# Optimization experiments

Measured on AMD Instinct MI355X. Metric: run time of the kernel, lower is better.

The kernel has to match this reference:

```python
import jax, jax.numpy as jnp
import numpy as np

N, E, SEQ, IN, HID, OUT = 2048, 65536, 5, 32, 64, 16
EPS = 1e-5


def setup_inputs() -> dict:
    ks = jax.random.split(jax.random.key(0), 16)
    def w(k, shape):
        return jax.random.normal(k, shape, jnp.float32) / np.float32(np.sqrt(shape[0]))
    z = lambda n: jnp.zeros((n,), jnp.float32)
    return dict(
        x=jax.random.normal(ks[0], (SEQ, N, IN), jnp.float32),
        edge_weight=jax.random.uniform(ks[1], (E,), jnp.float32),
        Wcz=w(ks[2], (IN, HID)), bcz=z(HID), Wlz=w(ks[3], (2 * HID, HID)), blz=z(HID),
        Wcr=w(ks[4], (IN, HID)), bcr=z(HID), Wlr=w(ks[5], (2 * HID, HID)), blr=z(HID),
        Wch=w(ks[6], (IN, HID)), bch=z(HID), Wlh=w(ks[7], (2 * HID, HID)), blh=z(HID),
        Wred=w(ks[8], (SEQ * HID, HID)), bred=z(HID),
        Wc1=w(ks[9], (HID, HID)), bc1=z(HID), Wc2=w(ks[10], (HID, HID)), bc2=z(HID),
        g1=jnp.ones((HID,), jnp.float32), be1=z(HID),
        g2=jnp.ones((HID,), jnp.float32), be2=z(HID),
        Wout=w(ks[11], (HID, OUT)), bout=z(OUT),
        Wi1=w(ks[12], (2 * HID, HID)), bi1=z(HID),
        Wi2=w(ks[13], (HID, 1)), bi2=z(1),
        edge_index=jax.random.randint(ks[14], (2, E), 0, N),
    )


def _layer_norm(h, g, b):
    mu = jnp.mean(h, -1, keepdims=True)
    var = jnp.mean((h - mu) ** 2, -1, keepdims=True)
    return (h - mu) * jax.lax.rsqrt(var + EPS) * g + b


def _forward(x, edge_weight, Wcz, bcz, Wlz, blz, Wcr, bcr, Wlr, blr,
             Wch, bch, Wlh, blh, Wred, bred, Wc1, bc1, Wc2, bc2,
             g1, be1, g2, be2, Wout, bout, Wi1, bi1, Wi2, bi2, edge_index):
    src, dst = edge_index[0], edge_index[1]
    # GCN symmetric normalization with self-loops (weight 1.0); shared by all convs.
    deg = jax.ops.segment_sum(edge_weight, dst, num_segments=N) + 1.0
    dinv = jax.lax.rsqrt(deg)
    norm = dinv[src] * edge_weight * dinv[dst]  # [E]
    dself = dinv * dinv                          # [N] self-loop coefficient

    def gcn(h, W, b):
        hw = h @ W
        agg = jax.ops.segment_sum(norm[:, None] * hw[src], dst, num_segments=N)
        return agg + dself[:, None] * hw + b

    # TGCN per timestep. The original passes no hidden state, so H resets to 0
    # each call: H_t = (1 - Z) * tanh(candidate); reset gate R is multiplied by
    # H=0 and has no effect (its params get zero gradient, matching torch).
    hs = []
    for t in range(SEQ):  # SEQ=5, fixed small loop
        Zg = jax.nn.sigmoid(gcn(x[t], Wcz, bcz) @ Wlz[:HID] + blz)
        Ht = jnp.tanh(gcn(x[t], Wch, bch) @ Wlh[:HID] + blh)
        hs.append((1.0 - Zg) * Ht)
    h = jnp.stack(hs, axis=1).reshape(N, SEQ * HID)
    h = h @ Wred + bred
    emb = h  # intermediate embeddings for the interaction predictor
    h = gcn(h, Wc1, bc1)
    h = jax.nn.relu(_layer_norm(h, g1, be1))  # dropout = identity in eval
    h = gcn(h, Wc2, bc2)
    h = jax.nn.relu(_layer_norm(h, g2, be2))
    node_pred = h @ Wout + bout
    # InteractionPredictor: cat([e_i, e_j]) @ Wi1 == e_i @ Wi1[:H] + e_j @ Wi1[H:]
    a = emb @ Wi1[:HID]
    bj = emb @ Wi1[HID:]
    hp = jax.nn.relu(a[:, None, :] + bj[None, :, :] + bi1)  # [N, N, HID]
    scores = (hp @ Wi2)[..., 0] + bi2[0]                     # [N, N]
    return node_pred, scores


def reference(x, edge_index, edge_weight, Wcz, bcz, Wlz, blz, Wcr, bcr, Wlr, blr,
              Wch, bch, Wlh, blh, Wred, bred, Wc1, bc1, Wc2, bc2,
              g1, be1, g2, be2, Wout, bout, Wi1, bi1, Wi2, bi2):
    return _forward(x, edge_weight, Wcz, bcz, Wlz, blz, Wcr, bcr, Wlr, blr,
                    Wch, bch, Wlh, blh, Wred, bred, Wc1, bc1, Wc2, bc2,
                    g1, be1, g2, be2, Wout, bout, Wi1, bi1, Wi2, bi2, edge_index)
```

## Files before the change

### kernel.cpp

```cpp
#include <hip/hip_runtime.h>
#include <math.h>

#define N_NODES 2048
#define N_EDGES 65536
#define SEQL 5
#define IN_F 32
#define HID 64
#define OUT_F 16
#define LN_EPS 1e-5f

__global__ __launch_bounds__(256) void k_deg_wcomb(
        const int* __restrict__ ei, const float* __restrict__ ew,
        const float* __restrict__ Wcz, const float* __restrict__ Wlz,
        const float* __restrict__ bcz, const float* __restrict__ blz,
        const float* __restrict__ Wch, const float* __restrict__ Wlh,
        const float* __restrict__ bch, const float* __restrict__ blh,
        float* __restrict__ deg, int* __restrict__ cnt,
        float* __restrict__ Wzp, float* __restrict__ Whp, float* __restrict__ bUV){
    int b = blockIdx.x, t = threadIdx.x;
    if (b < 256){
        int e = b * 256 + t;
        int d = ei[N_EDGES + e];
        atomicAdd(&deg[d], ew[e]);
        atomicAdd(&cnt[d], 1);
    } else {
        const float* Wc = (b == 256) ? Wcz : Wch;
        const float* Wl = (b == 256) ? Wlz : Wlh;
        const float* bc = (b == 256) ? bcz : bch;
        const float* bl = (b == 256) ? blz : blh;
        float* Wp = (b == 256) ? Wzp : Whp;
        for (int idx = t; idx < IN_F*HID; idx += 256){
            int i = idx >> 6, f = idx & 63;
            float s = 0.f;
            #pragma unroll 8
            for (int k = 0; k < HID; ++k) s += Wc[i*HID+k] * Wl[k*HID+f];
            Wp[idx] = s;
        }
        if (t < HID){
            float s = bl[t];
            for (int k = 0; k < HID; ++k) s += bc[k] * Wl[k*HID+t];
            bUV[(b-256)*HID + t] = s;
        }
    }
}

__global__ __launch_bounds__(1024) void k_scan(
        const float* __restrict__ deg, const int* __restrict__ cnt,
        int* __restrict__ rowptr, float* __restrict__ dinv, float* __restrict__ dself,
        int* __restrict__ fill){
    __shared__ int sc[1024];
    int t = threadIdx.x;
    int c0 = cnt[2*t], c1 = cnt[2*t+1];
    int ts = c0 + c1;
    sc[t] = ts;
    __syncthreads();
    for (int off = 1; off < 1024; off <<= 1){
        int v = (t >= off) ? sc[t - off] : 0;
        __syncthreads();
        sc[t] += v;
        __syncthreads();
    }
    int exc = sc[t] - ts;
    rowptr[2*t]   = exc;
    rowptr[2*t+1] = exc + c0;
    if (t == 1023) rowptr[N_NODES] = sc[t];
    float i0 = 1.f / sqrtf(deg[2*t] + 1.f);
    float i1 = 1.f / sqrtf(deg[2*t+1] + 1.f);
    dinv[2*t] = i0;     dinv[2*t+1] = i1;
    dself[2*t] = i0*i0; dself[2*t+1] = i1*i1;
    fill[2*t] = 0;      fill[2*t+1] = 0;
}

__global__ void k_csr(const int* __restrict__ ei, const float* __restrict__ ew,
                      const float* __restrict__ dinv, const int* __restrict__ rowptr,
                      int* __restrict__ fill, float2* __restrict__ cedge){
    int e = blockIdx.x * 256 + threadIdx.x;
    if (e < N_EDGES){
        int s = ei[e], d = ei[N_EDGES + e];
        int pos = rowptr[d] + atomicAdd(&fill[d], 1);
        float2 v;
        v.x = __int_as_float(s);
        v.y = dinv[s] * ew[e] * dinv[d];
        cedge[pos] = v;
    }
}

__global__ __launch_bounds__(320) void k_gate(const float* __restrict__ x,
        const float* __restrict__ dself, const int* __restrict__ rowptr,
        const float2* __restrict__ cedge,
        const float* __restrict__ bUV, const float* __restrict__ Wzp, const float* __restrict__ Whp,
        const float* __restrict__ Wred, const float* __restrict__ bred,
        const float* __restrict__ Wi1, const float* __restrict__ bi1, const float* __restrict__ Wc1,
        float* __restrict__ ag, float* __restrict__ bjp, float* __restrict__ hw1){
    int n = blockIdx.x;
    int tid = threadIdx.x;
    __shared__ float part[40*SEQL*IN_F];
    __shared__ float axs[SEQL][IN_F];
    __shared__ float hs[SEQL][HID];
    __shared__ float pw[SEQL][HID];
    __shared__ float hemb[HID];
    const int slot = tid >> 3, fl = tid & 7;
    const int f = tid & 63, t = tid >> 6;
    int beg = rowptr[n], end = rowptr[n+1];
    const float4* X4 = (const float4*)x;
    float4 a0 = {0,0,0,0}, a1 = {0,0,0,0}, a2 = {0,0,0,0}, a3 = {0,0,0,0}, a4 = {0,0,0,0};
    for (int p = beg + slot; p < end; p += 40){
        float2 ed = cedge[p];
        int s = __float_as_int(ed.x); float c = ed.y;
        float4 x0 = X4[(0*N_NODES + s)*8 + fl];
        float4 x1 = X4[(1*N_NODES + s)*8 + fl];
        float4 x2 = X4[(2*N_NODES + s)*8 + fl];
        float4 x3 = X4[(3*N_NODES + s)*8 + fl];
        float4 x4v= X4[(4*N_NODES + s)*8 + fl];
        a0.x += c*x0.x; a0.y += c*x0.y; a0.z += c*x0.z; a0.w += c*x0.w;
        a1.x += c*x1.x; a1.y += c*x1.y; a1.z += c*x1.z; a1.w += c*x1.w;
        a2.x += c*x2.x; a2.y += c*x2.y; a2.z += c*x2.z; a2.w += c*x2.w;
        a3.x += c*x3.x; a3.y += c*x3.y; a3.z += c*x3.z; a3.w += c*x3.w;
        a4.x += c*x4v.x; a4.y += c*x4v.y; a4.z += c*x4v.z; a4.w += c*x4v.w;
    }
    *(float4*)&part[(slot*SEQL + 0)*IN_F + fl*4] = a0;
    *(float4*)&part[(slot*SEQL + 1)*IN_F + fl*4] = a1;
    *(float4*)&part[(slot*SEQL + 2)*IN_F + fl*4] = a2;
    *(float4*)&part[(slot*SEQL + 3)*IN_F + fl*4] = a3;
    *(float4*)&part[(slot*SEQL + 4)*IN_F + fl*4] = a4;
    __syncthreads();
    if (tid < SEQL*IN_F){
        int tt = tid >> 5, ff = tid & 31;
        float s = dself[n] * x[(tt*N_NODES + n)*IN_F + ff];
        #pragma unroll 8
        for (int sl = 0; sl < 40; ++sl) s += part[(sl*SEQL + tt)*IN_F + ff];
        axs[tt][ff] = s;
    }
    __syncthreads();
    {
        float zz = bUV[f], hh = bUV[HID + f];
        #pragma unroll
        for (int i = 0; i < IN_F; ++i){
            float a = axs[t][i];
            zz += a * Wzp[i*HID + f];
            hh += a * Whp[i*HID + f];
        }
        float z = 1.f / (1.f + expf(-zz));
        hs[t][f] = (1.f - z) * tanhf(hh);
    }
    __syncthreads();
    {   float pp = 0.f;
        #pragma unroll
        for (int k = 0; k < HID; ++k) pp += hs[t][k] * Wred[(t*HID + k)*HID + f];
        pw[t][f] = pp;
    }
    __syncthreads();
    if (tid < HID){
        float hr = bred[tid];
        #pragma unroll
        for (int t2 = 0; t2 < SEQL; ++t2) hr += pw[t2][tid];
        hemb[tid] = hr;
    }
    __syncthreads();
    if (t < 3){
        const float* W = (t == 0) ? Wi1 : (t == 1) ? (Wi1 + HID*HID) : Wc1;
        float acc = (t == 1) ? bi1[f] : 0.f;
        #pragma unroll
        for (int k = 0; k < HID; ++k) acc += hemb[k] * W[k*HID + f];
        float* O = (t == 0) ? ag : (t == 1) ? bjp : hw1;
        O[n*HID + f] = acc;
    }
}

__global__ __launch_bounds__(512) void k_gcn1(
        const float* __restrict__ hw1, const float* __restrict__ dself,
        const int* __restrict__ rowptr, const float2* __restrict__ cedge,
        const float* __restrict__ bc1, const float* __restrict__ g1, const float* __restrict__ be1,
        const float* __restrict__ Wc2, float* __restrict__ hw2){
    int n = blockIdx.x;
    int tid = threadIdx.x;
    __shared__ float part[32*HID];
    __shared__ float hsh[HID];
    __shared__ float red8[8*HID];
    const int slot = tid >> 4, fl = tid & 15;
    const int f = tid & 63, w = tid >> 6;
    int beg = rowptr[n], end = rowptr[n+1];
    const float4* H4 = (const float4*)hw1;
    float4 acc = {0,0,0,0};
    for (int p = beg + slot; p < end; p += 32){
        float2 ed = cedge[p];
        int s = __float_as_int(ed.x); float c = ed.y;
        float4 h = H4[s*16 + fl];
        acc.x += c*h.x; acc.y += c*h.y; acc.z += c*h.z; acc.w += c*h.w;
    }
    *(float4*)&part[slot*HID + fl*4] = acc;
    __syncthreads();
    if (w == 0){
        float g = bc1[f] + dself[n] * hw1[n*HID + f];
        #pragma unroll 8
        for (int sl = 0; sl < 32; ++sl) g += part[sl*HID + f];
        float sum = g;
        for (int o = 32; o > 0; o >>= 1) sum += __shfl_xor(sum, o, 64);
        float mu = sum * (1.f/64.f);
        float d = g - mu;
        float vs = d * d;
        for (int o = 32; o > 0; o >>= 1) vs += __shfl_xor(vs, o, 64);
        float var = vs * (1.f/64.f);
        float h = d * (1.f / sqrtf(var + LN_EPS)) * g1[f] + be1[f];
        hsh[f] = fmaxf(h, 0.f);
    }
    __syncthreads();
    float s = 0.f;
    #pragma unroll
    for (int k = 0; k < 8; ++k) s += hsh[w*8 + k] * Wc2[(w*8 + k)*HID + f];
    red8[w*HID + f] = s;
    __syncthreads();
    if (w == 0){
        float o = 0.f;
        #pragma unroll
        for (int k = 0; k < 8; ++k) o += red8[k*HID + f];
        hw2[n*HID + f] = o;
    }
}

__global__ __launch_bounds__(512) void k_gcn2s(
        const float* __restrict__ hw2, const float* __restrict__ dself,
        const int* __restrict__ rowptr, const float2* __restrict__ cedge,
        const float* __restrict__ bc2, const float* __restrict__ g2, const float* __restrict__ be2,
        const float* __restrict__ Wout, const float* __restrict__ bout,
        const float* __restrict__ ag, const float* __restrict__ bjp,
        const float* __restrict__ Wi2, const float* __restrict__ bi2,
        float* __restrict__ outp, float* __restrict__ outs){
    int blk = blockIdx.x;
    int tid = threadIdx.x;
    if (blk < N_NODES){
        __shared__ float part[32*HID];
        __shared__ float hsh[HID];
        int n = blk;
        const int slot = tid >> 4, fl = tid & 15;
        const int f = tid & 63, w = tid >> 6;
        int beg = rowptr[n], end = rowptr[n+1];
        const float4* H4 = (const float4*)hw2;
        float4 acc = {0,0,0,0};
        for (int p = beg + slot; p < end; p += 32){
            float2 ed = cedge[p];
            int s = __float_as_int(ed.x); float c = ed.y;
            float4 h = H4[s*16 + fl];
            acc.x += c*h.x; acc.y += c*h.y; acc.z += c*h.z; acc.w += c*h.w;
        }
        *(float4*)&part[slot*HID + fl*4] = acc;
        __syncthreads();
        if (w == 0){
            float g = bc2[f] + dself[n] * hw2[n*HID + f];
            #pragma unroll 8
            for (int sl = 0; sl < 32; ++sl) g += part[sl*HID + f];
            float sum = g;
            for (int o = 32; o > 0; o >>= 1) sum += __shfl_xor(sum, o, 64);
            float mu = sum * (1.f/64.f);
            float d = g - mu;
            float vs = d * d;
            for (int o = 32; o > 0; o >>= 1) vs += __shfl_xor(vs, o, 64);
            float var = vs * (1.f/64.f);
            float h = d * (1.f / sqrtf(var + LN_EPS)) * g2[f] + be2[f];
            hsh[f] = fmaxf(h, 0.f);
        }
        __syncthreads();
        if (w == 0 && f < OUT_F){
            float s = bout[f];
            #pragma unroll
            for (int k = 0; k < HID; ++k) s += hsh[k] * Wout[k*OUT_F + f];
            outp[n*OUT_F + f] = s;
        }
    } else {
        __shared__ float bs[64*65];
        __shared__ float wv[64];
        int tl = blk - N_NODES;
        int j0 = (tl & 31) * 64;
        int i0 = (tl >> 5) * 32;
        for (int idx = tid; idx < 4096; idx += 512){
            int jj = idx >> 6, f = idx & 63;
            bs[jj*65 + f] = bjp[(j0 + jj)*HID + f];
        }
        if (tid < 64) wv[tid] = Wi2[tid];
        __syncthreads();
        int tj = tid & 63;
        int w = __builtin_amdgcn_readfirstlane(tid >> 6);
        const float* ar = ag + (i0 + w*4)*HID;
        float bi2v = bi2[0];
        float acc0 = 0.f, acc1 = 0.f, acc2 = 0.f, acc3 = 0.f;
        #pragma unroll
        for (int f = 0; f < 64; ++f){
            float bv = bs[tj*65 + f];
            float wf = wv[f];
            acc0 += fmaxf(ar[       f] + bv, 0.f) * wf;
            acc1 += fmaxf(ar[ 64 +  f] + bv, 0.f) * wf;
            acc2 += fmaxf(ar[128 +  f] + bv, 0.f) * wf;
            acc3 += fmaxf(ar[192 +  f] + bv, 0.f) * wf;
        }
        long ro = (long)(i0 + w*4) * N_NODES + j0 + tj;
        outs[ro                ] = acc0 + bi2v;
        outs[ro +     N_NODES  ] = acc1 + bi2v;
        outs[ro + 2L* N_NODES  ] = acc2 + bi2v;
        outs[ro + 3L* N_NODES  ] = acc3 + bi2v;
    }
}

extern "C" void kernel_launch(void* const* d_in, const int* in_sizes, int n_in,
                              void* d_out, int out_size, void* d_ws, size_t ws_size,
                              hipStream_t stream){
    const float* x   = (const float*)d_in[0];
    const float* ew  = (const float*)d_in[1];
    const float* Wcz = (const float*)d_in[2];  const float* bcz = (const float*)d_in[3];
    const float* Wlz = (const float*)d_in[4];  const float* blz = (const float*)d_in[5];
    const float* Wch = (const float*)d_in[10]; const float* bch = (const float*)d_in[11];
    const float* Wlh = (const float*)d_in[12]; const float* blh = (const float*)d_in[13];
    const float* Wred= (const float*)d_in[14]; const float* bred= (const float*)d_in[15];
    const float* Wc1 = (const float*)d_in[16]; const float* bc1 = (const float*)d_in[17];
    const float* Wc2 = (const float*)d_in[18]; const float* bc2 = (const float*)d_in[19];
    const float* g1  = (const float*)d_in[20]; const float* be1 = (const float*)d_in[21];
    const float* g2  = (const float*)d_in[22]; const float* be2 = (const float*)d_in[23];
    const float* Wout= (const float*)d_in[24]; const float* bout= (const float*)d_in[25];
    const float* Wi1 = (const float*)d_in[26]; const float* bi1 = (const float*)d_in[27];
    const float* Wi2 = (const float*)d_in[28]; const float* bi2 = (const float*)d_in[29];
    const int*  ei  = (const int*)d_in[30];

    float* w = (float*)d_ws;
    float* deg    = w;
    int*   cnt    = (int*)(w + 2048);
    int*   rowptr = (int*)(w + 4096);
    float* dinv   = w + 6656;
    float* dself  = w + 8704;
    int*   fill   = (int*)(w + 10752);
    float2* cedge = (float2*)(w + 12800);
    float* Wzp    = w + 143872;
    float* Whp    = w + 145920;
    float* bUV    = w + 147968;
    float* ag     = w + 148096;
    float* bjp    = w + 279168;
    float* hw1    = w + 410240;
    float* hw2    = w + 541312;

    hipMemsetAsync(deg, 0, 16384, stream);
    k_deg_wcomb<<<258, 256, 0, stream>>>(ei, ew, Wcz, Wlz, bcz, blz, Wch, Wlh, bch, blh,
                                         deg, cnt, Wzp, Whp, bUV);
    k_scan<<<1, 1024, 0, stream>>>(deg, cnt, rowptr, dinv, dself, fill);
    k_csr<<<N_EDGES/256, 256, 0, stream>>>(ei, ew, dinv, rowptr, fill, cedge);
    k_gate<<<N_NODES, 320, 0, stream>>>(x, dself, rowptr, cedge, bUV, Wzp, Whp,
                                        Wred, bred, Wi1, bi1, Wc1, ag, bjp, hw1);
    k_gcn1<<<N_NODES, 512, 0, stream>>>(hw1, dself, rowptr, cedge, bc1, g1, be1, Wc2, hw2);
    k_gcn2s<<<N_NODES + 2048, 512, 0, stream>>>(hw2, dself, rowptr, cedge,
                                                bc2, g2, be2, Wout, bout,
                                                ag, bjp, Wi2, bi2,
                                                (float*)d_out, (float*)d_out + N_NODES*OUT_F);
}
```

Measured before the change: 217.0 us.

## Retile pairwise score computation into 64x64 LDS tiles with register blocking

The interaction-score branch now stages both the row (ag) and column (bjp) embedding tiles in LDS, transposed so that each feature is contiguous across nodes. Each thread computes a 4x2 block of outputs instead of a 4x1 column strip, and the row operands no longer come from global memory per thread. Tiles grow from 32x64 to 64x64, which halves the number of score blocks. Outputs are written as float2. LDS use per block doubles and the stores become 8-byte strided writes.

Measured after the change: 226.3 us. +4.3%, slower.

```diff
diff --git a/kernel.cpp b/kernel.cpp
--- a/kernel.cpp
+++ b/kernel.cpp
@@ -267,36 +267,45 @@
             outp[n*OUT_F + f] = s;
         }
     } else {
-        __shared__ float bs[64*65];
+        __shared__ float at[64*65];
+        __shared__ float bt[64*65];
         __shared__ float wv[64];
         int tl = blk - N_NODES;
+        int i0 = (tl >> 5) * 64;
         int j0 = (tl & 31) * 64;
-        int i0 = (tl >> 5) * 32;
-        for (int idx = tid; idx < 4096; idx += 512){
-            int jj = idx >> 6, f = idx & 63;
-            bs[jj*65 + f] = bjp[(j0 + jj)*HID + f];
+        #pragma unroll
+        for (int k = 0; k < 8; ++k){
+            int idx = tid + k*512;
+            int r = idx >> 6, c = idx & 63;
+            at[c*65 + r] = ag [(i0 + r)*HID + c];
+            bt[c*65 + r] = bjp[(j0 + r)*HID + c];
         }
         if (tid < 64) wv[tid] = Wi2[tid];
         __syncthreads();
-        int tj = tid & 63;
-        int w = __builtin_amdgcn_readfirstlane(tid >> 6);
-        const float* ar = ag + (i0 + w*4)*HID;
+        const int ti = tid & 15;
+        const int jg = tid >> 4;
+        float acc[4][2] = {{0,0},{0,0},{0,0},{0,0}};
+        #pragma unroll 8
+        for (int f = 0; f < 64; ++f){
+            float wf = wv[f];
+            float b0 = bt[f*65 + 2*jg];
+            float b1 = bt[f*65 + 2*jg + 1];
+            #pragma unroll
+            for (int r = 0; r < 4; ++r){
+                float av = at[f*65 + 4*ti + r];
+                acc[r][0] = fmaf(fmaxf(av + b0, 0.f), wf, acc[r][0]);
+                acc[r][1] = fmaf(fmaxf(av + b1, 0.f), wf, acc[r][1]);
+            }
+        }
         float bi2v = bi2[0];
-        float acc0 = 0.f, acc1 = 0.f, acc2 = 0.f, acc3 = 0.f;
-        #pragma unroll
-        for (int f = 0; f < 64; ++f){
-            float bv = bs[tj*65 + f];
-            float wf = wv[f];
-            acc0 += fmaxf(ar[       f] + bv, 0.f) * wf;
-            acc1 += fmaxf(ar[ 64 +  f] + bv, 0.f) * wf;
-            acc2 += fmaxf(ar[128 +  f] + bv, 0.f) * wf;
-            acc3 += fmaxf(ar[192 +  f] + bv, 0.f) * wf;
-        }
-        long ro = (long)(i0 + w*4) * N_NODES + j0 + tj;
-        outs[ro                ] = acc0 + bi2v;
-        outs[ro +     N_NODES  ] = acc1 + bi2v;
-        outs[ro + 2L* N_NODES  ] = acc2 + bi2v;
-        outs[ro + 3L* N_NODES  ] = acc3 + bi2v;
+        #pragma unroll
+        for (int r = 0; r < 4; ++r){
+            long ro = (long)(i0 + 4*ti + r) * N_NODES + j0 + 2*jg;
+            float2 o;
+            o.x = acc[r][0] + bi2v;
+            o.y = acc[r][1] + bi2v;
+            *(float2*)&outs[ro] = o;
+        }
     }
 }
 
@@ -343,7 +352,7 @@
     k_gate<<<N_NODES, 320, 0, stream>>>(x, dself, rowptr, cedge, bUV, Wzp, Whp,
                                         Wred, bred, Wi1, bi1, Wc1, ag, bjp, hw1);
     k_gcn1<<<N_NODES, 512, 0, stream>>>(hw1, dself, rowptr, cedge, bc1, g1, be1, Wc2, hw2);
-    k_gcn2s<<<N_NODES + 2048, 512, 0, stream>>>(hw2, dself, rowptr, cedge,
+    k_gcn2s<<<N_NODES + 1024, 512, 0, stream>>>(hw2, dself, rowptr, cedge,
                                                 bc2, g2, be2, Wout, bout,
                                                 ag, bjp, Wi2, bi2,
                                                 (float*)d_out, (float*)d_out + N_NODES*OUT_F);
```
